# Performance work log

Measured on AMD Instinct MI355X. Metric: run time of the kernel, lower is better.

The kernel has to match this reference:

```python
import jax, jax.numpy as jnp
import numpy as np

POOL_H, POOL_W = 7, 7  # pool_shape from __init__
CANONICAL = 224.0     # FPN canonical box size


def _bilinear_one_image(img, ys, xs):
    """img: [H,W,C]; ys: [N,ph]; xs: [N,pw] -> [N,ph,pw,C].
    Matches tf.image.crop_and_resize bilinear sampling (boxes in-range)."""
    H, W, _ = img.shape
    y0f = jnp.floor(ys)
    x0f = jnp.floor(xs)
    wy = ys - y0f  # [N,ph]
    wx = xs - x0f  # [N,pw]
    y0 = jnp.clip(y0f.astype(jnp.int32), 0, H - 1)
    y1 = jnp.clip(y0 + 1, 0, H - 1)
    x0 = jnp.clip(x0f.astype(jnp.int32), 0, W - 1)
    x1 = jnp.clip(x0 + 1, 0, W - 1)
    tl = img[y0[:, :, None], x0[:, None, :]]  # [N,ph,pw,C]
    tr = img[y0[:, :, None], x1[:, None, :]]
    bl = img[y1[:, :, None], x0[:, None, :]]
    br = img[y1[:, :, None], x1[:, None, :]]
    wxe = wx[:, None, :, None]
    wye = wy[:, :, None, None]
    top = tl + (tr - tl) * wxe
    bot = bl + (br - bl) * wxe
    return top + (bot - top) * wye


def _crop_and_resize(fm, boxes):
    """fm: [B,H,W,C]; boxes: [B,N,4] normalized (y1,x1,y2,x2) -> [B,N,ph,pw,C]."""
    H, W = fm.shape[1], fm.shape[2]
    y1, x1, y2, x2 = (boxes[..., k] for k in range(4))
    ii = jnp.arange(POOL_H, dtype=boxes.dtype) / (POOL_H - 1)  # [ph]
    jj = jnp.arange(POOL_W, dtype=boxes.dtype) / (POOL_W - 1)  # [pw]
    ys = (y1[..., None] + ii * (y2 - y1)[..., None]) * (H - 1)  # [B,N,ph]
    xs = (x1[..., None] + jj * (x2 - x1)[..., None]) * (W - 1)  # [B,N,pw]
    return jax.vmap(_bilinear_one_image)(fm, ys, xs)


def reference(rois, img_metas, fm2, fm3, fm4, fm5):
    # rois: [B,N,4]; img_metas: [B,11]; fm_l: [B,H_l,W_l,C]
    boxes = jax.lax.stop_gradient(rois)  # original stop_gradients level_rois
    metas = jax.lax.stop_gradient(img_metas)
    pad_h = metas[:, 7]
    pad_w = metas[:, 8]
    area = (pad_h * pad_w)[:, None]  # [B,1]
    h = boxes[..., 2] - boxes[..., 0]
    w = boxes[..., 3] - boxes[..., 1]
    roi_level = jnp.log(jnp.sqrt(h * w) / (CANONICAL / jnp.sqrt(area))) / jnp.log(2.0)
    roi_level = jnp.clip(4 + jnp.round(roi_level).astype(jnp.int32), 2, 5)  # [B,N]
    B, N = boxes.shape[0], boxes.shape[1]
    C = fm2.shape[-1]
    out = jnp.zeros((B, N, POOL_H, POOL_W, C), fm2.dtype)
    for lvl, fm in zip((2, 3, 4, 5), (fm2, fm3, fm4, fm5)):
        pooled = _crop_and_resize(fm, boxes)  # [B,N,ph,pw,C]
        out = jnp.where((roi_level == lvl)[..., None, None, None], pooled, out)
    return out


def setup_inputs() -> dict:
    key = jax.random.key(0)
    k1, k2, k3, k4, k5, k6, k7, k8 = jax.random.split(key, 8)
    B, N = 2, 1000
    # valid normalized boxes: y1,x1 in [0,0.6), h,w in [0.02,0.4)
    y1 = jax.random.uniform(k1, (B, N), minval=0.0, maxval=0.6)
    x1 = jax.random.uniform(k2, (B, N), minval=0.0, maxval=0.6)
    hh = jax.random.uniform(k3, (B, N), minval=0.02, maxval=0.4)
    ww = jax.random.uniform(k4, (B, N), minval=0.02, maxval=0.4)
    rois = jnp.stack([y1, x1, jnp.minimum(y1 + hh, 1.0), jnp.minimum(x1 + ww, 1.0)], axis=-1).astype(jnp.float32)
    img_metas = jnp.zeros((B, 11), jnp.float32).at[:, 7].set(1024.0).at[:, 8].set(1024.0)
    fm2 = jax.random.normal(k5, (B, 256, 256, 256), jnp.float32)
    fm3 = jax.random.normal(k6, (B, 128, 128, 256), jnp.float32)
    fm4 = jax.random.normal(k7, (B, 64, 64, 256), jnp.float32)
    fm5 = jax.random.normal(k8, (B, 32, 32, 256), jnp.float32)
    return {"rois": rois, "img_metas": img_metas, "fm2": fm2, "fm3": fm3, "fm4": fm4, "fm5": fm5}
```

## Files before the change

### kernel.cpp

```cpp
#include <hip/hip_runtime.h>
#include <math.h>

#define POOL 7
#define CCH 256
#define CANON 224.0f

typedef float nfloat4 __attribute__((ext_vector_type(4)));

__device__ __forceinline__ nfloat4 f4_blend(nfloat4 a, nfloat4 b, float w) {
    return a + (b - a) * w;
}

__device__ __forceinline__ int roi_level(const float* __restrict__ rois,
                                         const float* __restrict__ metas,
                                         int idx, int N) {
    const int b = idx / N;
    const float* box = rois + (size_t)idx * 4;
    const float h = box[2] - box[0];
    const float w = box[3] - box[1];
    const float pad_h = metas[b * 11 + 7];
    const float pad_w = metas[b * 11 + 8];
    const float area = pad_h * pad_w;
    const float lvlf = logf(sqrtf(h * w) / (CANON / sqrtf(area))) / logf(2.0f);
    int lvl = 4 + (int)rintf(lvlf);
    return lvl < 2 ? 2 : (lvl > 5 ? 5 : lvl);
}

__global__ __launch_bounds__(1024) void bucket_kernel(
    const float* __restrict__ rois, const float* __restrict__ metas,
    int B, int N, int* __restrict__ perm)
{
    __shared__ int counts[64];
    __shared__ int offs[64];
    const int total = B * N;
    const int tid = threadIdx.x;
    if (tid < 64) counts[tid] = 0;
    __syncthreads();

    for (int i = tid; i < total; i += 1024) {
        const int b = i / N;
        const int lvl = roi_level(rois, metas, i, N);
        const float yc = 0.5f * (rois[(size_t)i * 4 + 0] + rois[(size_t)i * 4 + 2]);
        int band = (int)(yc * 8.0f); band = band < 0 ? 0 : (band > 7 ? 7 : band);
        const int key = b * 32 + (lvl - 2) * 8 + band;
        atomicAdd(&counts[key], 1);
    }
    __syncthreads();
    if (tid == 0) {
        int acc = 0;
        for (int k = 0; k < 64; ++k) { offs[k] = acc; acc += counts[k]; }
    }
    __syncthreads();
    for (int i = tid; i < total; i += 1024) {
        const int b = i / N;
        const int lvl = roi_level(rois, metas, i, N);
        const float yc = 0.5f * (rois[(size_t)i * 4 + 0] + rois[(size_t)i * 4 + 2]);
        int band = (int)(yc * 8.0f); band = band < 0 ? 0 : (band > 7 ? 7 : band);
        const int key = b * 32 + (lvl - 2) * 8 + band;
        const int pos = atomicAdd(&offs[key], 1);
        perm[pos] = i | (lvl << 24);
    }
}

__global__ __launch_bounds__(256) void roi_align_kernel(
    const float* __restrict__ rois,
    const float* __restrict__ fm2,
    const float* __restrict__ fm3,
    const float* __restrict__ fm4,
    const float* __restrict__ fm5,
    const int* __restrict__ perm,
    float* __restrict__ out,
    int B, int N)
{
    const int total = B * N;
    const int q = total >> 3, r = total & 7;
    const int k = blockIdx.x & 7, j = blockIdx.x >> 3;
    const int p = (k < r) ? k * (q + 1) + j : r * (q + 1) + (k - r) * q + j;

    const int e = perm[p];
    const int idx = e & 0xFFFFFF;
    const int lvl = e >> 24;
    const int b = idx / N;

    const float* box = rois + (size_t)idx * 4;
    const float y1 = box[0], x1 = box[1], y2 = box[2], x2 = box[3];
    const float h = y2 - y1;
    const float w = x2 - x1;

    const float* fm;
    int H, W;
    if (lvl == 2)      { fm = fm2; H = 256; W = 256; }
    else if (lvl == 3) { fm = fm3; H = 128; W = 128; }
    else if (lvl == 4) { fm = fm4; H = 64;  W = 64;  }
    else               { fm = fm5; H = 32;  W = 32;  }
    const float* img = fm + (size_t)b * H * W * CCH;

    const int tid  = threadIdx.x;
    const int wave = tid >> 6;
    const int lane = tid & 63;

    nfloat4* outp = (nfloat4*)(out + (size_t)idx * (POOL * POOL * CCH));

    const float Hm1 = (float)(H - 1);
    const float Wm1 = (float)(W - 1);

#pragma unroll 4
    for (int it = 0; it < 13; ++it) {
        int pp = wave + it * 4;
        pp = pp > 48 ? 48 : pp;
        const int i = pp / POOL;
        const int jx = pp % POOL;
        const float ii = (float)i / 6.0f;
        const float jj = (float)jx / 6.0f;
        const float ys = (y1 + ii * h) * Hm1;
        const float xs = (x1 + jj * w) * Wm1;

        const float y0f = floorf(ys);
        const float x0f = floorf(xs);
        const float wy = ys - y0f;
        const float wx = xs - x0f;

        int y0 = (int)y0f; y0 = y0 < 0 ? 0 : (y0 > H - 1 ? H - 1 : y0);
        int x0 = (int)x0f; x0 = x0 < 0 ? 0 : (x0 > W - 1 ? W - 1 : x0);
        int y1i = y0 + 1;  y1i = y1i > H - 1 ? H - 1 : y1i;
        int x1i = x0 + 1;  x1i = x1i > W - 1 ? W - 1 : x1i;

        const nfloat4* tl = (const nfloat4*)(img + ((size_t)(y0  * W + x0 )) * CCH) + lane;
        const nfloat4* tr = (const nfloat4*)(img + ((size_t)(y0  * W + x1i)) * CCH) + lane;
        const nfloat4* bl = (const nfloat4*)(img + ((size_t)(y1i * W + x0 )) * CCH) + lane;
        const nfloat4* br = (const nfloat4*)(img + ((size_t)(y1i * W + x1i)) * CCH) + lane;

        const nfloat4 vtl = *tl;
        const nfloat4 vtr = *tr;
        const nfloat4 vbl = *bl;
        const nfloat4 vbr = *br;

        const nfloat4 top = f4_blend(vtl, vtr, wx);
        const nfloat4 bot = f4_blend(vbl, vbr, wx);
        const nfloat4 res = f4_blend(top, bot, wy);

        __builtin_nontemporal_store(res, &outp[pp * 64 + lane]);
    }
}

extern "C" void kernel_launch(void* const* d_in, const int* in_sizes, int n_in,
                              void* d_out, int out_size, void* d_ws, size_t ws_size,
                              hipStream_t stream) {
    const float* rois  = (const float*)d_in[0];
    const float* metas = (const float*)d_in[1];
    const float* fm2   = (const float*)d_in[2];
    const float* fm3   = (const float*)d_in[3];
    const float* fm4   = (const float*)d_in[4];
    const float* fm5   = (const float*)d_in[5];
    float* out = (float*)d_out;
    int* perm = (int*)d_ws;

    const int B = in_sizes[1] / 11;
    const int N = in_sizes[0] / (4 * B);

    bucket_kernel<<<1, 1024, 0, stream>>>(rois, metas, B, N, perm);
    roi_align_kernel<<<B * N, 256, 0, stream>>>(rois, fm2, fm3, fm4, fm5,
                                                perm, out, B, N);
}
```

Baseline: 41.20 us.

## Restructure ROI align to wave-per-row and cache bucket keys in LDS

Result: faster. 38.69 us (-6.1%).

```diff
diff --git a/kernel.cpp b/kernel.cpp
--- a/kernel.cpp
+++ b/kernel.cpp
@@ -4,18 +4,15 @@
 #define POOL 7
 #define CCH 256
 #define CANON 224.0f
+#define MAX_LDS_KEYS 8192
 
 typedef float nfloat4 __attribute__((ext_vector_type(4)));
 
-__device__ __forceinline__ nfloat4 f4_blend(nfloat4 a, nfloat4 b, float w) {
-    return a + (b - a) * w;
-}
-
-__device__ __forceinline__ int roi_level(const float* __restrict__ rois,
-                                         const float* __restrict__ metas,
-                                         int idx, int N) {
-    const int b = idx / N;
-    const float* box = rois + (size_t)idx * 4;
+__device__ __forceinline__ int roi_level_of(const float* __restrict__ rois,
+                                            const float* __restrict__ metas,
+                                            int i, int N) {
+    const int b = i / N;
+    const float* box = rois + (size_t)i * 4;
     const float h = box[2] - box[0];
     const float w = box[3] - box[1];
     const float pad_h = metas[b * 11 + 7];
@@ -26,43 +23,64 @@
     return lvl < 2 ? 2 : (lvl > 5 ? 5 : lvl);
 }
 
+__device__ __forceinline__ int bucket_key(const float* __restrict__ rois,
+                                          const float* __restrict__ metas,
+                                          int i, int N, int* lvl_out) {
+    const int lvl = roi_level_of(rois, metas, i, N);
+    *lvl_out = lvl;
+    const float yc = 0.5f * (rois[(size_t)i * 4 + 0] + rois[(size_t)i * 4 + 2]);
+    int band = (int)(yc * 16.0f); band = band < 0 ? 0 : (band > 15 ? 15 : band);
+    const int b = i / N;
+    return ((b & 1) * 64) + (lvl - 2) * 16 + band;
+}
+
 __global__ __launch_bounds__(1024) void bucket_kernel(
     const float* __restrict__ rois, const float* __restrict__ metas,
     int B, int N, int* __restrict__ perm)
 {
-    __shared__ int counts[64];
-    __shared__ int offs[64];
+    __shared__ int counts[128];
+    __shared__ int offs[128];
+    __shared__ int excl[128];
+    __shared__ unsigned short keys[MAX_LDS_KEYS];
     const int total = B * N;
     const int tid = threadIdx.x;
-    if (tid < 64) counts[tid] = 0;
+    const bool cache = (total <= MAX_LDS_KEYS);
+
+    if (tid < 128) counts[tid] = 0;
     __syncthreads();
 
     for (int i = tid; i < total; i += 1024) {
-        const int b = i / N;
-        const int lvl = roi_level(rois, metas, i, N);
-        const float yc = 0.5f * (rois[(size_t)i * 4 + 0] + rois[(size_t)i * 4 + 2]);
-        int band = (int)(yc * 8.0f); band = band < 0 ? 0 : (band > 7 ? 7 : band);
-        const int key = b * 32 + (lvl - 2) * 8 + band;
+        int lvl;
+        const int key = bucket_key(rois, metas, i, N, &lvl);
+        if (cache) keys[i] = (unsigned short)(key | (lvl << 8));
         atomicAdd(&counts[key], 1);
     }
     __syncthreads();
-    if (tid == 0) {
-        int acc = 0;
-        for (int k = 0; k < 64; ++k) { offs[k] = acc; acc += counts[k]; }
+
+    if (tid < 128) offs[tid] = counts[tid];
+    __syncthreads();
+    for (int d = 1; d < 128; d <<= 1) {
+        int v = 0;
+        if (tid < 128 && tid >= d) v = offs[tid - d];
+        __syncthreads();
+        if (tid < 128 && tid >= d) offs[tid] += v;
+        __syncthreads();
     }
+    if (tid < 128) excl[tid] = (tid == 0) ? 0 : offs[tid - 1];
     __syncthreads();
+    if (tid < 128) offs[tid] = excl[tid];
+    __syncthreads();
+
     for (int i = tid; i < total; i += 1024) {
-        const int b = i / N;
-        const int lvl = roi_level(rois, metas, i, N);
-        const float yc = 0.5f * (rois[(size_t)i * 4 + 0] + rois[(size_t)i * 4 + 2]);
-        int band = (int)(yc * 8.0f); band = band < 0 ? 0 : (band > 7 ? 7 : band);
-        const int key = b * 32 + (lvl - 2) * 8 + band;
+        int key, lvl;
+        if (cache) { const int e = keys[i]; key = e & 0xFF; lvl = e >> 8; }
+        else       { key = bucket_key(rois, metas, i, N, &lvl); }
         const int pos = atomicAdd(&offs[key], 1);
         perm[pos] = i | (lvl << 24);
     }
 }
 
-__global__ __launch_bounds__(256) void roi_align_kernel(
+__global__ __launch_bounds__(448) void roi_align_kernel(
     const float* __restrict__ rois,
     const float* __restrict__ fm2,
     const float* __restrict__ fm3,
@@ -74,8 +92,8 @@
 {
     const int total = B * N;
     const int q = total >> 3, r = total & 7;
-    const int k = blockIdx.x & 7, j = blockIdx.x >> 3;
-    const int p = (k < r) ? k * (q + 1) + j : r * (q + 1) + (k - r) * q + j;
+    const int k = blockIdx.x & 7, jb = blockIdx.x >> 3;
+    const int p = (k < r) ? k * (q + 1) + jb : r * (q + 1) + (k - r) * q + jb;
 
     const int e = perm[p];
     const int idx = e & 0xFFFFFF;
@@ -95,51 +113,43 @@
     else               { fm = fm5; H = 32;  W = 32;  }
     const float* img = fm + (size_t)b * H * W * CCH;
 
-    const int tid  = threadIdx.x;
-    const int wave = tid >> 6;
-    const int lane = tid & 63;
-
-    nfloat4* outp = (nfloat4*)(out + (size_t)idx * (POOL * POOL * CCH));
+    const int wave = threadIdx.x >> 6;
+    const int lane = threadIdx.x & 63;
 
     const float Hm1 = (float)(H - 1);
     const float Wm1 = (float)(W - 1);
 
-#pragma unroll 4
-    for (int it = 0; it < 13; ++it) {
-        int pp = wave + it * 4;
-        pp = pp > 48 ? 48 : pp;
-        const int i = pp / POOL;
-        const int jx = pp % POOL;
-        const float ii = (float)i / 6.0f;
-        const float jj = (float)jx / 6.0f;
-        const float ys = (y1 + ii * h) * Hm1;
+    const float ii = (float)wave / 6.0f;
+    const float ys = (y1 + ii * h) * Hm1;
+    const float y0f = floorf(ys);
+    const float wy = ys - y0f;
+    int y0 = (int)y0f; y0 = y0 < 0 ? 0 : (y0 > H - 1 ? H - 1 : y0);
+    int y1i = y0 + 1;  y1i = y1i > H - 1 ? H - 1 : y1i;
+
+    const nfloat4* rowT = (const nfloat4*)(img + (size_t)y0  * W * CCH) + lane;
+    const nfloat4* rowB = (const nfloat4*)(img + (size_t)y1i * W * CCH) + lane;
+    nfloat4* outp = (nfloat4*)(out + (size_t)idx * (POOL * POOL * CCH))
+                    + wave * (POOL * 64) + lane;
+
+#pragma unroll
+    for (int j = 0; j < POOL; ++j) {
+        const float jj = (float)j / 6.0f;
         const float xs = (x1 + jj * w) * Wm1;
-
-        const float y0f = floorf(ys);
         const float x0f = floorf(xs);
-        const float wy = ys - y0f;
         const float wx = xs - x0f;
-
-        int y0 = (int)y0f; y0 = y0 < 0 ? 0 : (y0 > H - 1 ? H - 1 : y0);
         int x0 = (int)x0f; x0 = x0 < 0 ? 0 : (x0 > W - 1 ? W - 1 : x0);
-        int y1i = y0 + 1;  y1i = y1i > H - 1 ? H - 1 : y1i;
         int x1i = x0 + 1;  x1i = x1i > W - 1 ? W - 1 : x1i;
 
-        const nfloat4* tl = (const nfloat4*)(img + ((size_t)(y0  * W + x0 )) * CCH) + lane;
-        const nfloat4* tr = (const nfloat4*)(img + ((size_t)(y0  * W + x1i)) * CCH) + lane;
-        const nfloat4* bl = (const nfloat4*)(img + ((size_t)(y1i * W + x0 )) * CCH) + lane;
-        const nfloat4* br = (const nfloat4*)(img + ((size_t)(y1i * W + x1i)) * CCH) + lane;
+        const nfloat4 vtl = rowT[(size_t)x0  * 64];
+        const nfloat4 vtr = rowT[(size_t)x1i * 64];
+        const nfloat4 vbl = rowB[(size_t)x0  * 64];
+        const nfloat4 vbr = rowB[(size_t)x1i * 64];
 
-        const nfloat4 vtl = *tl;
-        const nfloat4 vtr = *tr;
-        const nfloat4 vbl = *bl;
-        const nfloat4 vbr = *br;
+        const nfloat4 top = vtl + (vtr - vtl) * wx;
+        const nfloat4 bot = vbl + (vbr - vbl) * wx;
+        const nfloat4 res = top + (bot - top) * wy;
 
-        const nfloat4 top = f4_blend(vtl, vtr, wx);
-        const nfloat4 bot = f4_blend(vbl, vbr, wx);
-        const nfloat4 res = f4_blend(top, bot, wy);
-
-        __builtin_nontemporal_store(res, &outp[pp * 64 + lane]);
+        __builtin_nontemporal_store(res, outp + j * 64);
     }
 }
 
@@ -159,6 +169,6 @@
     const int N = in_sizes[0] / (4 * B);
 
     bucket_kernel<<<1, 1024, 0, stream>>>(rois, metas, B, N, perm);
-    roi_align_kernel<<<B * N, 256, 0, stream>>>(rois, fm2, fm3, fm4, fm5,
+    roi_align_kernel<<<B * N, 448, 0, stream>>>(rois, fm2, fm3, fm4, fm5,
                                                 perm, out, B, N);
 }
```
